# Kernel optimization log

Hardware: AMD Instinct MI355X
Metric: run time of the kernel (lower is better)

Reference implementation:

```python
import jax, jax.numpy as jnp
import numpy as np


def setup_inputs() -> dict:
    key = jax.random.key(0)
    kq, kk, kv = jax.random.split(key, 3)
    B, H, N, D = 2, 16, 2048, 128
    q = jax.random.normal(kq, (B, H, N, D), dtype=jnp.float32)
    k = jax.random.normal(kk, (B, H, N, D), dtype=jnp.float32)
    v = jax.random.normal(kv, (B, H, N, D), dtype=jnp.float32)
    return {"q": q, "k": k, "v": v, "num_sink": 4, "window_size": 1024}


def reference(q, k, v, num_sink, window_size):
    # Sink + sliding-window causal attention (single-device path of the SP wrapper).
    # Query i attends to key j iff j <= i AND (j < num_sink OR i - j < window_size).
    B, H, N, D = q.shape
    scale = 1.0 / np.sqrt(D).astype(np.float32)
    i = jnp.arange(N)[:, None]   # query positions
    j = jnp.arange(N)[None, :]   # key positions
    mask = (j <= i) & ((j < num_sink) | ((i - j) < window_size))  # [N, N]
    scores = jnp.einsum('bhid,bhjd->bhij', q, k) * scale          # [B,H,N,N]
    scores = jnp.where(mask, scores, jnp.finfo(scores.dtype).min)
    attn = jax.nn.softmax(scores, axis=-1)
    return jnp.einsum('bhij,bhjd->bhid', attn, v)
```

## Files before the change

kernel.cpp:

```cpp
#include <hip/hip_runtime.h>
#include <stdint.h>

#define NN 2048
#define DD 128
#define BHH 32
#define QT 64
#define KT 64

typedef short v8s __attribute__((ext_vector_type(8)));
typedef short v4s __attribute__((ext_vector_type(4)));
typedef float v4f __attribute__((ext_vector_type(4)));

__device__ __forceinline__ unsigned short f2bf(float x) {
  unsigned u = __builtin_bit_cast(unsigned, x);
  u += 0x7fffu + ((u >> 16) & 1u);
  return (unsigned short)(u >> 16);
}

__device__ __forceinline__ v8s cvt8(const float* __restrict__ p) {
  v8s r;
#pragma unroll
  for (int j = 0; j < 8; j++) r[j] = (short)f2bf(p[j]);
  return r;
}

__global__ void vtranspose(const float* __restrict__ V, unsigned short* __restrict__ Vt) {
  __shared__ unsigned short t[64 * 68];
  const int bh = blockIdx.z;
  const int n0 = blockIdx.x * 64, d0 = blockIdx.y * 64;
  const int tid = threadIdx.x;
  const float* src = V + ((size_t)bh * NN + n0) * DD + d0;
#pragma unroll
  for (int p = 0; p < 4; p++) {
    int r = p * 16 + (tid >> 4);
    int c = (tid & 15) * 4;
    v4f f = *(const v4f*)(src + (size_t)r * DD + c);
    v4s u;
#pragma unroll
    for (int j = 0; j < 4; j++) u[j] = (short)f2bf(f[j]);
    *(v4s*)(t + r * 68 + c) = u;
  }
  __syncthreads();
  unsigned short* dst = Vt + ((size_t)bh * DD + d0) * NN + n0;
#pragma unroll
  for (int p = 0; p < 2; p++) {
    int d = p * 32 + (tid >> 3);
    int nc = (tid & 7) * 8;
    v8s o;
#pragma unroll
    for (int j = 0; j < 8; j++) o[j] = (short)t[(nc + j) * 68 + d];
    *(v8s*)(dst + (size_t)d * NN + nc) = o;
  }
}

template <bool USE_VT>
__global__ __launch_bounds__(256, 4) void attn(
    const float* __restrict__ Q, const float* __restrict__ Kf,
    const unsigned short* __restrict__ Vt, const float* __restrict__ Vf,
    const int* __restrict__ nsp, const int* __restrict__ wsp,
    float* __restrict__ O) {
  const int ns = nsp[0], win = wsp[0];
  const int bh = blockIdx.x;
  const int q0 = (gridDim.y - 1 - blockIdx.y) * QT;
  const int tid = threadIdx.x;
  const int w = tid >> 6;
  const int l = tid & 63;
  const int lo = l & 15, q4 = l >> 4;

  __shared__ __align__(16) unsigned short Kl[KT * DD];
  __shared__ __align__(16) unsigned short Vl[KT * DD];
  __shared__ __align__(16) unsigned short Pl[4 * 16 * KT];

  v8s qf[4];
  {
    const float* qb = Q + ((size_t)bh * NN + q0 + w * 16 + lo) * DD + q4 * 8;
#pragma unroll
    for (int kc = 0; kc < 4; kc++) qf[kc] = cvt8(qb + kc * 32);
  }

  float lsum[4];
  v4f oa[8];
#pragma unroll
  for (int r = 0; r < 4; r++) lsum[r] = 0.f;
#pragma unroll
  for (int nc = 0; nc < 8; nc++) oa[nc] = (v4f){0.f, 0.f, 0.f, 0.f};

  const float csc = 0.088388347648318447f * 1.4426950408889634f;

  const size_t koff0 = ((size_t)bh * NN + w * 16 + lo) * DD + q4 * 8;
  unsigned short* Pw = Pl + w * 1024;
  const int qrow0 = q0 + w * 16;
  const int rb = q4 * 4;

  for (int kb = 0; kb < q0 + QT; kb += KT) {
    if ((kb >= ns) && (kb + KT - 1 < q0 - win + 1)) continue;

    v8s kst[4];
    {
      const float* g = Kf + koff0 + (size_t)kb * DD;
#pragma unroll
      for (int kc = 0; kc < 4; kc++) kst[kc] = cvt8(g + kc * 32);
    }
    v8s vst[4];
    if (USE_VT) {
#pragma unroll
      for (int i = 0; i < 4; i++) {
        int f = w * 4 + i, kt = f >> 3, nc = f & 7;
        vst[i] = *(const v8s*)(Vt + ((size_t)bh * DD + nc * 16 + lo) * NN + kb +
                               kt * 32 + q4 * 8);
      }
    }

    __syncthreads();
#pragma unroll
    for (int kc = 0; kc < 4; kc++)
      *(v8s*)(Kl + (w * 4 + kc) * 512 + l * 8) = kst[kc];
    if (USE_VT) {
#pragma unroll
      for (int i = 0; i < 4; i++)
        *(v8s*)(Vl + (w * 4 + i) * 512 + l * 8) = vst[i];
    }
    __syncthreads();

    v4f s[4];
#pragma unroll
    for (int ct = 0; ct < 4; ct++) {
      s[ct] = (v4f){0.f, 0.f, 0.f, 0.f};
#pragma unroll
      for (int kc = 0; kc < 4; kc++) {
        v8s kf = *(const v8s*)(Kl + (ct * 4 + kc) * 512 + l * 8);
        s[ct] = __builtin_amdgcn_mfma_f32_16x16x32_bf16(qf[kc], kf, s[ct], 0, 0, 0);
      }
    }
#pragma unroll
    for (int ct = 0; ct < 4; ct++) {
      int kj = kb + ct * 16 + lo;
#pragma unroll
      for (int r = 0; r < 4; r++) {
        int qi = qrow0 + rb + r;
        bool valid = (kj <= qi) && ((kj < ns) || (qi - kj < win));
        s[ct][r] = valid ? __builtin_amdgcn_exp2f(s[ct][r] * csc) : 0.f;
      }
    }
#pragma unroll
    for (int r = 0; r < 4; r++)
      lsum[r] += (s[0][r] + s[1][r]) + (s[2][r] + s[3][r]);

#pragma unroll
    for (int ct = 0; ct < 4; ct++) {
#pragma unroll
      for (int r = 0; r < 4; r++) {
        int row = rb + r;
        int idx = (ct >> 1) * 512 + (row + 16 * ((ct & 1) * 2 + ((l >> 3) & 1))) * 8 + (l & 7);
        Pw[idx] = f2bf(s[ct][r]);
      }
    }
#pragma unroll
    for (int kt = 0; kt < 2; kt++) {
      v8s pf = *(const v8s*)(Pw + kt * 512 + l * 8);
#pragma unroll
      for (int nc = 0; nc < 8; nc++) {
        v8s vf;
        if (USE_VT) {
          vf = *(const v8s*)(Vl + (kt * 8 + nc) * 512 + l * 8);
        } else {
#pragma unroll
          for (int j = 0; j < 8; j++) {
            size_t vi = ((size_t)bh * NN + kb + kt * 32 + q4 * 8 + j) * DD + nc * 16 + lo;
            vf[j] = (short)f2bf(Vf[vi]);
          }
        }
        oa[nc] = __builtin_amdgcn_mfma_f32_16x16x32_bf16(pf, vf, oa[nc], 0, 0, 0);
      }
    }
  }

  float inv[4];
#pragma unroll
  for (int r = 0; r < 4; r++) {
    float v = lsum[r];
    v += __shfl_xor(v, 1, 64);
    v += __shfl_xor(v, 2, 64);
    v += __shfl_xor(v, 4, 64);
    v += __shfl_xor(v, 8, 64);
    inv[r] = 1.f / v;
  }
  float* ob = O + ((size_t)bh * NN + qrow0) * DD;
#pragma unroll
  for (int nc = 0; nc < 8; nc++)
#pragma unroll
    for (int r = 0; r < 4; r++)
      ob[(size_t)(rb + r) * DD + nc * 16 + lo] = oa[nc][r] * inv[r];
}

extern "C" void kernel_launch(void* const* d_in, const int* in_sizes, int n_in,
                              void* d_out, int out_size, void* d_ws, size_t ws_size,
                              hipStream_t stream) {
  const float* q = (const float*)d_in[0];
  const float* k = (const float*)d_in[1];
  const float* v = (const float*)d_in[2];
  const int* nsp = (const int*)d_in[3];
  const int* wsp = (const int*)d_in[4];
  float* out = (float*)d_out;

  const size_t vt_bytes = (size_t)BHH * NN * DD * sizeof(unsigned short);
  if (ws_size >= vt_bytes) {
    unsigned short* vt = (unsigned short*)d_ws;
    vtranspose<<<dim3(NN / 64, DD / 64, BHH), 256, 0, stream>>>(v, vt);
    attn<true><<<dim3(BHH, NN / QT), 256, 0, stream>>>(q, k, vt, v, nsp, wsp, out);
  } else {
    attn<false><<<dim3(BHH, NN / QT), 256, 0, stream>>>(q, k, nullptr, v, nsp, wsp, out);
  }
}
```

Baseline: 226.6 us.

## Pair short and long query tiles per block and precast K to bf16

Blocks now process one or two query tiles. Tiles with q-index 16 to 31 run alone, and tiles 0 to 15 are paired with the tile at 15-p. This balances the causal and sliding-window work across the grid and shrinks the grid to 768 blocks. A prep kernel also converts K to bf16 in the workspace alongside the V transpose, so the attention loop loads half the K bytes and skips per-iteration conversion. The cost is an extra pass over K and twice the workspace, and the paired blocks run their two tiles serially.

```diff
diff --git a/kernel.cpp b/kernel.cpp
--- a/kernel.cpp
+++ b/kernel.cpp
@@ -6,6 +6,7 @@
 #define BHH 32
 #define QT 64
 #define KT 64
+#define NQT (NN / QT)
 
 typedef short v8s __attribute__((ext_vector_type(8)));
 typedef short v4s __attribute__((ext_vector_type(4)));
@@ -24,11 +25,22 @@
   return r;
 }
 
-__global__ void vtranspose(const float* __restrict__ V, unsigned short* __restrict__ Vt) {
+__global__ void prep(const float* __restrict__ K, const float* __restrict__ V,
+                     unsigned short* __restrict__ Kb, unsigned short* __restrict__ Vt) {
+  const int z = blockIdx.z;
+  const int tid = threadIdx.x;
+  if (z >= BHH) {
+    const int bh = z - BHH;
+    const int chunk = blockIdx.y * 32 + blockIdx.x;
+    size_t base = (size_t)bh * NN * DD + (size_t)chunk * 4096 + (size_t)tid * 16;
+#pragma unroll
+    for (int h = 0; h < 2; h++)
+      *(v8s*)(Kb + base + h * 8) = cvt8(K + base + h * 8);
+    return;
+  }
   __shared__ unsigned short t[64 * 68];
-  const int bh = blockIdx.z;
+  const int bh = z;
   const int n0 = blockIdx.x * 64, d0 = blockIdx.y * 64;
-  const int tid = threadIdx.x;
   const float* src = V + ((size_t)bh * NN + n0) * DD + d0;
 #pragma unroll
   for (int p = 0; p < 4; p++) {
@@ -53,15 +65,21 @@
   }
 }
 
-template <bool USE_VT>
+template <bool KBF, bool USE_VT>
 __global__ __launch_bounds__(256, 4) void attn(
-    const float* __restrict__ Q, const float* __restrict__ Kf,
+    const float* __restrict__ Q,
+    const float* __restrict__ Kf, const unsigned short* __restrict__ Kb,
     const unsigned short* __restrict__ Vt, const float* __restrict__ Vf,
     const int* __restrict__ nsp, const int* __restrict__ wsp,
     float* __restrict__ O) {
   const int ns = nsp[0], win = wsp[0];
-  const int bh = blockIdx.x;
-  const int q0 = (gridDim.y - 1 - blockIdx.y) * QT;
+  const int j = blockIdx.x;
+  const int bh = j & 31;
+  const int jobid = j >> 5;
+  int qis[2], njobs;
+  if (jobid < 16) { njobs = 1; qis[0] = 31 - jobid; qis[1] = 0; }
+  else { int p = jobid - 16; njobs = 2; qis[0] = 15 - p; qis[1] = p; }
+
   const int tid = threadIdx.x;
   const int w = tid >> 6;
   const int l = tid & 63;
@@ -71,126 +89,131 @@
   __shared__ __align__(16) unsigned short Vl[KT * DD];
   __shared__ __align__(16) unsigned short Pl[4 * 16 * KT];
 
-  v8s qf[4];
-  {
-    const float* qb = Q + ((size_t)bh * NN + q0 + w * 16 + lo) * DD + q4 * 8;
-#pragma unroll
-    for (int kc = 0; kc < 4; kc++) qf[kc] = cvt8(qb + kc * 32);
-  }
-
-  float lsum[4];
-  v4f oa[8];
-#pragma unroll
-  for (int r = 0; r < 4; r++) lsum[r] = 0.f;
-#pragma unroll
-  for (int nc = 0; nc < 8; nc++) oa[nc] = (v4f){0.f, 0.f, 0.f, 0.f};
-
   const float csc = 0.088388347648318447f * 1.4426950408889634f;
-
-  const size_t koff0 = ((size_t)bh * NN + w * 16 + lo) * DD + q4 * 8;
   unsigned short* Pw = Pl + w * 1024;
-  const int qrow0 = q0 + w * 16;
   const int rb = q4 * 4;
 
-  for (int kb = 0; kb < q0 + QT; kb += KT) {
-    if ((kb >= ns) && (kb + KT - 1 < q0 - win + 1)) continue;
-
-    v8s kst[4];
+  for (int ji = 0; ji < njobs; ji++) {
+    const int q0 = qis[ji] * QT;
+    const int qrow0 = q0 + w * 16;
+
+    v8s qf[4];
     {
-      const float* g = Kf + koff0 + (size_t)kb * DD;
-#pragma unroll
-      for (int kc = 0; kc < 4; kc++) kst[kc] = cvt8(g + kc * 32);
+      const float* qb = Q + ((size_t)bh * NN + qrow0 + lo) * DD + q4 * 8;
+#pragma unroll
+      for (int kc = 0; kc < 4; kc++) qf[kc] = cvt8(qb + kc * 32);
     }
-    v8s vst[4];
-    if (USE_VT) {
-#pragma unroll
-      for (int i = 0; i < 4; i++) {
-        int f = w * 4 + i, kt = f >> 3, nc = f & 7;
-        vst[i] = *(const v8s*)(Vt + ((size_t)bh * DD + nc * 16 + lo) * NN + kb +
-                               kt * 32 + q4 * 8);
+
+    float lsum[4];
+    v4f oa[8];
+#pragma unroll
+    for (int r = 0; r < 4; r++) lsum[r] = 0.f;
+#pragma unroll
+    for (int nc = 0; nc < 8; nc++) oa[nc] = (v4f){0.f, 0.f, 0.f, 0.f};
+
+    const size_t koff0 = ((size_t)bh * NN + w * 16 + lo) * DD + q4 * 8;
+
+    for (int kb = 0; kb < q0 + QT; kb += KT) {
+      if ((kb >= ns) && (kb + KT - 1 < q0 - win + 1)) continue;
+
+      v8s kst[4];
+      {
+        size_t g = koff0 + (size_t)kb * DD;
+#pragma unroll
+        for (int kc = 0; kc < 4; kc++)
+          kst[kc] = KBF ? *(const v8s*)(Kb + g + kc * 32) : cvt8(Kf + g + kc * 32);
+      }
+      v8s vst[4];
+      if (USE_VT) {
+#pragma unroll
+        for (int i = 0; i < 4; i++) {
+          int f = w * 4 + i, kt = f >> 3, nc = f & 7;
+          vst[i] = *(const v8s*)(Vt + ((size_t)bh * DD + nc * 16 + lo) * NN + kb +
+                                 kt * 32 + q4 * 8);
+        }
+      }
+
+      __syncthreads();
+#pragma unroll
+      for (int kc = 0; kc < 4; kc++)
+        *(v8s*)(Kl + (w * 4 + kc) * 512 + l * 8) = kst[kc];
+      if (USE_VT) {
+#pragma unroll
+        for (int i = 0; i < 4; i++)
+          *(v8s*)(Vl + (w * 4 + i) * 512 + l * 8) = vst[i];
+      }
+      __syncthreads();
+
+      v4f s[4];
+#pragma unroll
+      for (int ct = 0; ct < 4; ct++) {
+        s[ct] = (v4f){0.f, 0.f, 0.f, 0.f};
+#pragma unroll
+        for (int kc = 0; kc < 4; kc++) {
+          v8s kf = *(const v8s*)(Kl + (ct * 4 + kc) * 512 + l * 8);
+          s[ct] = __builtin_amdgcn_mfma_f32_16x16x32_bf16(qf[kc], kf, s[ct], 0, 0, 0);
+        }
+      }
+#pragma unroll
+      for (int ct = 0; ct < 4; ct++) {
+        int kj = kb + ct * 16 + lo;
+#pragma unroll
+        for (int r = 0; r < 4; r++) {
+          int qi = qrow0 + rb + r;
+          bool valid = (kj <= qi) && ((kj < ns) || (qi - kj < win));
+          s[ct][r] = valid ? __builtin_amdgcn_exp2f(s[ct][r] * csc) : 0.f;
+        }
+      }
+#pragma unroll
+      for (int r = 0; r < 4; r++)
+        lsum[r] += (s[0][r] + s[1][r]) + (s[2][r] + s[3][r]);
+
+#pragma unroll
+      for (int ct = 0; ct < 4; ct++) {
+#pragma unroll
+        for (int r = 0; r < 4; r++) {
+          int row = rb + r;
+          int idx = (ct >> 1) * 512 + (row + 16 * ((ct & 1) * 2 + ((l >> 3) & 1))) * 8 + (l & 7);
+          Pw[idx] = f2bf(s[ct][r]);
+        }
+      }
+#pragma unroll
+      for (int kt = 0; kt < 2; kt++) {
+        v8s pf = *(const v8s*)(Pw + kt * 512 + l * 8);
+#pragma unroll
+        for (int nc = 0; nc < 8; nc++) {
+          v8s vf;
+          if (USE_VT) {
+            vf = *(const v8s*)(Vl + (kt * 8 + nc) * 512 + l * 8);
+          } else {
+#pragma unroll
+            for (int jj = 0; jj < 8; jj++) {
+              size_t vi = ((size_t)bh * NN + kb + kt * 32 + q4 * 8 + jj) * DD + nc * 16 + lo;
+              vf[jj] = (short)f2bf(Vf[vi]);
+            }
+          }
+          oa[nc] = __builtin_amdgcn_mfma_f32_16x16x32_bf16(pf, vf, oa[nc], 0, 0, 0);
+        }
       }
     }
 
-    __syncthreads();
-#pragma unroll
-    for (int kc = 0; kc < 4; kc++)
-      *(v8s*)(Kl + (w * 4 + kc) * 512 + l * 8) = kst[kc];
-    if (USE_VT) {
-#pragma unroll
-      for (int i = 0; i < 4; i++)
-        *(v8s*)(Vl + (w * 4 + i) * 512 + l * 8) = vst[i];
+    float inv[4];
+#pragma unroll
+    for (int r = 0; r < 4; r++) {
+      float v = lsum[r];
+      v += __shfl_xor(v, 1, 64);
+      v += __shfl_xor(v, 2, 64);
+      v += __shfl_xor(v, 4, 64);
+      v += __shfl_xor(v, 8, 64);
+      inv[r] = 1.f / v;
     }
-    __syncthreads();
-
-    v4f s[4];
-#pragma unroll
-    for (int ct = 0; ct < 4; ct++) {
-      s[ct] = (v4f){0.f, 0.f, 0.f, 0.f};
-#pragma unroll
-      for (int kc = 0; kc < 4; kc++) {
-        v8s kf = *(const v8s*)(Kl + (ct * 4 + kc) * 512 + l * 8);
-        s[ct] = __builtin_amdgcn_mfma_f32_16x16x32_bf16(qf[kc], kf, s[ct], 0, 0, 0);
-      }
-    }
-#pragma unroll
-    for (int ct = 0; ct < 4; ct++) {
-      int kj = kb + ct * 16 + lo;
-#pragma unroll
-      for (int r = 0; r < 4; r++) {
-        int qi = qrow0 + rb + r;
-        bool valid = (kj <= qi) && ((kj < ns) || (qi - kj < win));
-        s[ct][r] = valid ? __builtin_amdgcn_exp2f(s[ct][r] * csc) : 0.f;
-      }
-    }
-#pragma unroll
-    for (int r = 0; r < 4; r++)
-      lsum[r] += (s[0][r] + s[1][r]) + (s[2][r] + s[3][r]);
-
-#pragma unroll
-    for (int ct = 0; ct < 4; ct++) {
-#pragma unroll
-      for (int r = 0; r < 4; r++) {
-        int row = rb + r;
-        int idx = (ct >> 1) * 512 + (row + 16 * ((ct & 1) * 2 + ((l >> 3) & 1))) * 8 + (l & 7);
-        Pw[idx] = f2bf(s[ct][r]);
-      }
-    }
-#pragma unroll
-    for (int kt = 0; kt < 2; kt++) {
-      v8s pf = *(const v8s*)(Pw + kt * 512 + l * 8);
-#pragma unroll
-      for (int nc = 0; nc < 8; nc++) {
-        v8s vf;
-        if (USE_VT) {
-          vf = *(const v8s*)(Vl + (kt * 8 + nc) * 512 + l * 8);
-        } else {
-#pragma unroll
-          for (int j = 0; j < 8; j++) {
-            size_t vi = ((size_t)bh * NN + kb + kt * 32 + q4 * 8 + j) * DD + nc * 16 + lo;
-            vf[j] = (short)f2bf(Vf[vi]);
-          }
-        }
-        oa[nc] = __builtin_amdgcn_mfma_f32_16x16x32_bf16(pf, vf, oa[nc], 0, 0, 0);
-      }
-    }
-  }
-
-  float inv[4];
-#pragma unroll
-  for (int r = 0; r < 4; r++) {
-    float v = lsum[r];
-    v += __shfl_xor(v, 1, 64);
-    v += __shfl_xor(v, 2, 64);
-    v += __shfl_xor(v, 4, 64);
-    v += __shfl_xor(v, 8, 64);
-    inv[r] = 1.f / v;
-  }
-  float* ob = O + ((size_t)bh * NN + qrow0) * DD;
-#pragma unroll
-  for (int nc = 0; nc < 8; nc++)
-#pragma unroll
-    for (int r = 0; r < 4; r++)
-      ob[(size_t)(rb + r) * DD + nc * 16 + lo] = oa[nc][r] * inv[r];
+    float* ob = O + ((size_t)bh * NN + qrow0) * DD;
+#pragma unroll
+    for (int nc = 0; nc < 8; nc++)
+#pragma unroll
+      for (int r = 0; r < 4; r++)
+        ob[(size_t)(rb + r) * DD + nc * 16 + lo] = oa[nc][r] * inv[r];
+  }
 }
 
 extern "C" void kernel_launch(void* const* d_in, const int* in_sizes, int n_in,
@@ -203,12 +226,18 @@
   const int* wsp = (const int*)d_in[4];
   float* out = (float*)d_out;
 
-  const size_t vt_bytes = (size_t)BHH * NN * DD * sizeof(unsigned short);
-  if (ws_size >= vt_bytes) {
-    unsigned short* vt = (unsigned short*)d_ws;
-    vtranspose<<<dim3(NN / 64, DD / 64, BHH), 256, 0, stream>>>(v, vt);
-    attn<true><<<dim3(BHH, NN / QT), 256, 0, stream>>>(q, k, vt, v, nsp, wsp, out);
+  const size_t half = (size_t)BHH * NN * DD * sizeof(unsigned short);
+  unsigned short* kbf = (unsigned short*)d_ws;
+  unsigned short* vt = (unsigned short*)((char*)d_ws + half);
+  const int nblocks = BHH * 24;
+
+  if (ws_size >= 2 * half) {
+    prep<<<dim3(32, 2, 2 * BHH), 256, 0, stream>>>(k, v, kbf, vt);
+    attn<true, true><<<nblocks, 256, 0, stream>>>(q, k, kbf, vt, v, nsp, wsp, out);
+  } else if (ws_size >= half) {
+    prep<<<dim3(32, 2, BHH), 256, 0, stream>>>(k, v, nullptr, (unsigned short*)d_ws);
+    attn<false, true><<<nblocks, 256, 0, stream>>>(q, k, nullptr, (unsigned short*)d_ws, v, nsp, wsp, out);
   } else {
-    attn<false><<<dim3(BHH, NN / QT), 256, 0, stream>>>(q, k, nullptr, v, nsp, wsp, out);
-  }
-}
+    attn<false, false><<<nblocks, 256, 0, stream>>>(q, k, nullptr, nullptr, v, nsp, wsp, out);
+  }
+}
```

Measured after the change: 199.0 us. 12.2% less time.
